# Kernel optimization log

Measured on AMD Instinct MI355X. Metric: run time of the kernel, lower is better.

## Reference

```python
import jax, jax.numpy as jnp
import numpy as np

EPS = 1e-6


def setup_inputs() -> dict:
    key = jax.random.key(0)
    ks = jax.random.split(key, 7)
    T, B, D, N = 512, 32, 1024, 128
    scale_w = (6.0 / (N + D)) ** 0.5  # xavier_uniform bound
    def w(k):
        return jax.random.uniform(k, (N, D), jnp.float32, -scale_w, scale_w)
    return {
        "x": jax.random.normal(ks[0], (T, B, D), jnp.float32),
        "S0": jnp.zeros((B, N, N), jnp.float32),
        "W_k": w(ks[1]),
        "W_v": w(ks[2]),
        "W_q": w(ks[3]),
        "W_erase": w(ks[4]),
        "W_write": w(ks[5]),
    }


def _ntm_forward(x, S0, W_k, W_v, W_q, W_erase, W_write):
    # Projections for all timesteps at once: (T, B, n_state)
    k = jnp.einsum('tbd,nd->tbn', x, W_k)
    v = jnp.einsum('tbd,nd->tbn', x, W_v)
    q = jnp.einsum('tbd,nd->tbn', x, W_q)
    erase = jnp.einsum('tbd,nd->tbn', x, W_erase)  # use_sigmoid=False: raw
    write = jnp.einsum('tbd,nd->tbn', x, W_write)

    def step(S, inp):
        k_t, v_t, q_t, e_t, w_t = inp
        k_norm = k_t / (jnp.linalg.norm(k_t, axis=-1, keepdims=True) + EPS)
        # S: (B, n, n); outer products via broadcasting
        erase_outer = e_t[:, :, None] * k_norm[:, None, :]
        write_outer = (w_t * v_t)[:, :, None] * k_norm[:, None, :]
        S_new = jnp.tanh(S * (1.0 - erase_outer) + write_outer)
        Sq = jnp.einsum('bij,bj->bi', S_new, q_t)
        out = Sq * jax.nn.silu(Sq)
        return S_new, out

    S_final, outputs = jax.lax.scan(step, S0, (k, v, q, erase, write))
    return outputs, S_final


def reference(x, S0, W_k, W_v, W_q, W_erase, W_write):
    return _ntm_forward(x, S0, W_k, W_v, W_q, W_erase, W_write)
```

## Files before the change

kernel.cpp:

```cpp
#include <hip/hip_runtime.h>
#include <hip/hip_bf16.h>


typedef __attribute__((ext_vector_type(8))) short bf16x8;
typedef __attribute__((ext_vector_type(4))) float f32x4;
typedef __attribute__((ext_vector_type(2))) float f32x2;
typedef __attribute__((ext_vector_type(4))) unsigned short u16x4;
typedef __attribute__((ext_vector_type(8))) unsigned short u16x8;

static constexpr int T_STEPS = 512;
static constexpr int BATCH   = 32;
static constexpr int DDIM    = 1024;
static constexpr int NDIM    = 128;
static constexpr int LDC     = 5 * NDIM;
static constexpr int MROWS   = T_STEPS * BATCH;
static constexpr int OUT_N   = T_STEPS * BATCH * NDIM;

static constexpr size_t C_BYTES = (size_t)MROWS * LDC * 4;

__device__ __forceinline__ unsigned short rne_bf16(float v) {
    unsigned u = __builtin_bit_cast(unsigned, v);
    u += 0x7FFFu + ((u >> 16) & 1u);
    return (unsigned short)(u >> 16);
}

__global__ __launch_bounds__(256) void wconv_kernel(
    const float* __restrict__ w0, const float* __restrict__ w1,
    const float* __restrict__ w2, const float* __restrict__ w3,
    const float* __restrict__ w4,
    unsigned short* __restrict__ W2)
{
    const int idx = blockIdx.x * 256 + threadIdx.x;
    const size_t e = (size_t)idx * 4;
    const int bn = (int)(e >> 17);
    const int r  = (int)(e & 131071);
    const int n  = r >> 10;
    const int k  = r & 1023;

    const float* wp = w0;
    if (bn == 1) wp = w1;
    else if (bn == 2) wp = w2;
    else if (bn == 3) wp = w3;
    else if (bn == 4) wp = w4;

    f32x4 v = *(const f32x4*)(wp + r);
    u16x4 h;
#pragma unroll
    for (int j = 0; j < 4; ++j) h[j] = rne_bf16(v[j]);

    const int kk   = k >> 5;
    const int quad = (k >> 3) & 3;
    const size_t off = ((((size_t)(bn * 32 + kk) * 128 + n) * 4 + quad) * 8) + (k & 7);
    *(u16x4*)(W2 + off) = h;
}

__global__ __launch_bounds__(512, 2) void gemm4_kernel(
    const float* __restrict__ x,
    const unsigned short* __restrict__ W2,
    float* __restrict__ C)
{
    __shared__ unsigned short lds[64 * 1024];

    const int m0   = blockIdx.x * 64;
    const int tid  = threadIdx.x;
    const int wave = tid >> 6, lane = tid & 63;
    const int quad = lane >> 4, l16 = lane & 15;

    {
        const int k8 = tid & 127;
        const int rb = tid >> 7;
#pragma unroll 4
        for (int it = 0; it < 16; ++it) {
            const int row = it * 4 + rb;
            const float* src = x + (size_t)(m0 + row) * DDIM + k8 * 8;
            f32x4 v0 = *(const f32x4*)src;
            f32x4 v1 = *(const f32x4*)(src + 4);
            u16x8 h;
            h[0] = rne_bf16(v0[0]); h[1] = rne_bf16(v0[1]);
            h[2] = rne_bf16(v0[2]); h[3] = rne_bf16(v0[3]);
            h[4] = rne_bf16(v1[0]); h[5] = rne_bf16(v1[1]);
            h[6] = rne_bf16(v1[2]); h[7] = rne_bf16(v1[3]);
            const int byteo = row * 2048 + ((k8 * 16) ^ ((row & 7) << 4));
            *(u16x8*)((char*)lds + byteo) = h;
        }
    }
    __syncthreads();

    f32x4 acc[5][4];
#pragma unroll
    for (int bn = 0; bn < 5; ++bn)
#pragma unroll
        for (int mi = 0; mi < 4; ++mi) acc[bn][mi] = (f32x4)(0.0f);

    const int aswz = (l16 & 7) << 4;
    const unsigned short* bp = W2 + ((size_t)((wave * 16 + l16) * 4 + quad)) * 8;

    auto LDA = [&](int mi, int kk) -> bf16x8 {
        const int byteo = (mi * 16 + l16) * 2048 + ((kk * 64 + quad * 16) ^ aswz);
        return *(const bf16x8*)((const char*)lds + byteo);
    };

    bf16x8 aC[4], bC[5], aN[4], bN[5];
#pragma unroll
    for (int mi = 0; mi < 4; ++mi) aC[mi] = LDA(mi, 0);
#pragma unroll
    for (int bn = 0; bn < 5; ++bn)
        bC[bn] = *(const bf16x8*)(bp + (size_t)bn * 131072);

    for (int kk = 0; kk < 32; kk += 2) {
#pragma unroll
        for (int mi = 0; mi < 4; ++mi) aN[mi] = LDA(mi, kk + 1);
#pragma unroll
        for (int bn = 0; bn < 5; ++bn)
            bN[bn] = *(const bf16x8*)(bp + (size_t)bn * 131072 + (size_t)(kk + 1) * 4096);
#pragma unroll
        for (int bn = 0; bn < 5; ++bn)
#pragma unroll
            for (int mi = 0; mi < 4; ++mi)
                acc[bn][mi] = __builtin_amdgcn_mfma_f32_16x16x32_bf16(
                    aC[mi], bC[bn], acc[bn][mi], 0, 0, 0);
        if (kk < 30) {
#pragma unroll
            for (int mi = 0; mi < 4; ++mi) aC[mi] = LDA(mi, kk + 2);
#pragma unroll
            for (int bn = 0; bn < 5; ++bn)
                bC[bn] = *(const bf16x8*)(bp + (size_t)bn * 131072 + (size_t)(kk + 2) * 4096);
        }
#pragma unroll
        for (int bn = 0; bn < 5; ++bn)
#pragma unroll
            for (int mi = 0; mi < 4; ++mi)
                acc[bn][mi] = __builtin_amdgcn_mfma_f32_16x16x32_bf16(
                    aN[mi], bN[bn], acc[bn][mi], 0, 0, 0);
    }

#pragma unroll
    for (int bn = 0; bn < 5; ++bn)
#pragma unroll
        for (int mi = 0; mi < 4; ++mi) {
            const int rw = m0 + mi * 16 + quad * 4;
            const int cl = bn * 128 + wave * 16 + l16;
#pragma unroll
            for (int r = 0; r < 4; ++r)
                C[(size_t)(rw + r) * LDC + cl] = acc[bn][mi][r];
        }
}

__global__ __launch_bounds__(256) void knorm_kernel(float* __restrict__ C)
{
    const int r    = blockIdx.x * 4 + (threadIdx.x >> 6);
    const int lane = threadIdx.x & 63;
    float* base = C + (size_t)r * LDC;

    f32x2 k2 = *(const f32x2*)(base + lane * 2);
    f32x2 v2 = *(const f32x2*)(base + NDIM + lane * 2);
    f32x2 w2 = *(const f32x2*)(base + 4 * NDIM + lane * 2);

    float ss = k2.x * k2.x + k2.y * k2.y;
#pragma unroll
    for (int off = 32; off >= 1; off >>= 1) ss += __shfl_xor(ss, off, 64);
    float inv = __builtin_amdgcn_rcpf(sqrtf(ss) + 1e-6f);

    f32x2 kn = {k2.x * inv, k2.y * inv};
    f32x2 wv = {v2.x * w2.x, v2.y * w2.y};
    *(f32x2*)(base + lane * 2) = kn;
    *(f32x2*)(base + NDIM + lane * 2) = wv;
}

__device__ __forceinline__ float tanh_fast(float xx) {
    float ex = __builtin_amdgcn_exp2f(xx * 2.8853900817779268f);
    float r  = __builtin_amdgcn_rcpf(ex + 1.0f);
    return fmaf(-2.0f, r, 1.0f);
}

template <int CTRL, int RMASK>
__device__ __forceinline__ float dpp_add(float x) {
    int yi = __builtin_amdgcn_update_dpp(
        0, __builtin_bit_cast(int, x), CTRL, RMASK, 0xF, true);
    return x + __builtin_bit_cast(float, yi);
}

__device__ __forceinline__ float dpp_reduce32(float x) {
    x = dpp_add<0xB1,  0xF>(x);
    x = dpp_add<0x4E,  0xF>(x);
    x = dpp_add<0x141, 0xF>(x);
    x = dpp_add<0x140, 0xF>(x);
    x = dpp_add<0x142, 0xA>(x);
    return x;
}

__global__ __launch_bounds__(256) void ntm_scan_kernel(
    const float* __restrict__ C, const float* __restrict__ S0,
    float* __restrict__ out)
{
    const int L    = blockIdx.x;
    const int b    = (L & 7) + 8 * ((L >> 3) & 3);
    const int row  = (L >> 5) * 8 + (threadIdx.x >> 5);
    const int g    = threadIdx.x & 31;
    const int col0 = g * 4;

    f32x4 S = *(const f32x4*)(S0 + ((size_t)b * NDIM + row) * NDIM + col0);

    const size_t STRIDE = (size_t)BATCH * LDC;
    const float* pb = C + (size_t)b * LDC;

    f32x4 kS[4], qS[4];
    float eS[4], wvS[4];

#pragma unroll
    for (int s = 0; s < 2; ++s) {
        const float* p = pb + (size_t)s * STRIDE;
        kS[s]  = *(const f32x4*)(p + col0);
        qS[s]  = *(const f32x4*)(p + 2 * NDIM + col0);
        eS[s]  = p[3 * NDIM + row];
        wvS[s] = p[NDIM + row];
    }

    float* op = out + (size_t)b * NDIM + row;

    for (int ti = 0; ti < T_STEPS / 4; ++ti) {
#pragma unroll
        for (int j = 0; j < 4; ++j) {
            const int t = ti * 4 + j;
            {
                int tp = t + 2;
                if (tp > T_STEPS - 1) tp = T_STEPS - 1;
                const float* p = pb + (size_t)tp * STRIDE;
                const int ps = (j + 2) & 3;
                kS[ps]  = *(const f32x4*)(p + col0);
                qS[ps]  = *(const f32x4*)(p + 2 * NDIM + col0);
                eS[ps]  = p[3 * NDIM + row];
                wvS[ps] = p[NDIM + row];
            }
            float dot = 0.0f;
#pragma unroll
            for (int u = 0; u < 4; ++u) {
                float t0  = fmaf(-eS[j], S[u], wvS[j]);
                float pre = fmaf(kS[j][u], t0, S[u]);
                S[u] = tanh_fast(pre);
                dot = fmaf(S[u], qS[j][u], dot);
            }
            dot = dpp_reduce32(dot);

            if ((threadIdx.x & 31) == 31) {
                const float d = dot;
                const float sg = __builtin_amdgcn_rcpf(
                    1.0f + __builtin_amdgcn_exp2f(-d * 1.4426950408889634f));
                op[(size_t)t * BATCH * NDIM] = d * d * sg;
            }
        }
    }

    *(f32x4*)(out + (size_t)T_STEPS * BATCH * NDIM
              + ((size_t)b * NDIM + row) * NDIM + col0) = S;
}

extern "C" void kernel_launch(void* const* d_in, const int* in_sizes, int n_in,
                              void* d_out, int out_size, void* d_ws, size_t ws_size,
                              hipStream_t stream) {
    const float* x  = (const float*)d_in[0];
    const float* S0 = (const float*)d_in[1];
    const float* wk = (const float*)d_in[2];
    const float* wv = (const float*)d_in[3];
    const float* wq = (const float*)d_in[4];
    const float* we = (const float*)d_in[5];
    const float* ww = (const float*)d_in[6];
    float* out = (float*)d_out;
    float* C   = (float*)d_ws;
    unsigned short* W2 = (unsigned short*)((char*)d_ws + C_BYTES);

    wconv_kernel<<<640, 256, 0, stream>>>(wk, wv, wq, we, ww, W2);
    gemm4_kernel<<<256, 512, 0, stream>>>(x, W2, C);
    knorm_kernel<<<MROWS / 4, 256, 0, stream>>>(C);
    ntm_scan_kernel<<<512, 256, 0, stream>>>(C, S0, out);
}
```

Measured before the change: 266.5 us.

## Split GEMM into column passes, move SiLU out of scan, simplify scan indexing

The projection GEMM now runs three sequential passes over 2, 2 and 1 column blocks, which cuts accumulator registers per pass at the cost of re-reading A from LDS three times. The scan kernel drops the per-step SiLU transcendental and the clamped prefetch index. It walks a running pointer instead and peels the last four steps, and it gets a two-blocks-per-SM launch bound. A separate elementwise kernel then applies d*d*sigmoid(d) to all outputs, which adds one extra read and write pass over the output.

```diff
diff --git a/kernel.cpp b/kernel.cpp
--- a/kernel.cpp
+++ b/kernel.cpp
@@ -54,7 +54,74 @@
     *(u16x4*)(W2 + off) = h;
 }
 
-__global__ __launch_bounds__(512, 2) void gemm4_kernel(
+template<int BN0, int NB>
+__device__ __forceinline__ void gemm_pass(
+    const unsigned short (&lds)[64 * 1024],
+    const unsigned short* __restrict__ bp,
+    float* __restrict__ C,
+    int m0, int wave, int quad, int l16, int aswz)
+{
+    auto LDA = [&](int mi, int kk) -> bf16x8 {
+        const int byteo = (mi * 16 + l16) * 2048 + ((kk * 64 + quad * 16) ^ aswz);
+        return *(const bf16x8*)((const char*)lds + byteo);
+    };
+
+    f32x4 acc[NB][4];
+#pragma unroll
+    for (int q = 0; q < NB; ++q)
+#pragma unroll
+        for (int mi = 0; mi < 4; ++mi) acc[q][mi] = (f32x4)(0.0f);
+
+    const unsigned short* bpp[NB];
+#pragma unroll
+    for (int q = 0; q < NB; ++q) bpp[q] = bp + (size_t)(BN0 + q) * 131072;
+
+    bf16x8 aC[4], bC[NB], aN[4], bN[NB];
+#pragma unroll
+    for (int mi = 0; mi < 4; ++mi) aC[mi] = LDA(mi, 0);
+#pragma unroll
+    for (int q = 0; q < NB; ++q) bC[q] = *(const bf16x8*)bpp[q];
+
+    for (int kk = 0; kk < 32; kk += 2) {
+#pragma unroll
+        for (int mi = 0; mi < 4; ++mi) aN[mi] = LDA(mi, kk + 1);
+#pragma unroll
+        for (int q = 0; q < NB; ++q)
+            bN[q] = *(const bf16x8*)(bpp[q] + (size_t)(kk + 1) * 4096);
+#pragma unroll
+        for (int q = 0; q < NB; ++q)
+#pragma unroll
+            for (int mi = 0; mi < 4; ++mi)
+                acc[q][mi] = __builtin_amdgcn_mfma_f32_16x16x32_bf16(
+                    aC[mi], bC[q], acc[q][mi], 0, 0, 0);
+        if (kk < 30) {
+#pragma unroll
+            for (int mi = 0; mi < 4; ++mi) aC[mi] = LDA(mi, kk + 2);
+#pragma unroll
+            for (int q = 0; q < NB; ++q)
+                bC[q] = *(const bf16x8*)(bpp[q] + (size_t)(kk + 2) * 4096);
+        }
+#pragma unroll
+        for (int q = 0; q < NB; ++q)
+#pragma unroll
+            for (int mi = 0; mi < 4; ++mi)
+                acc[q][mi] = __builtin_amdgcn_mfma_f32_16x16x32_bf16(
+                    aN[mi], bN[q], acc[q][mi], 0, 0, 0);
+    }
+
+#pragma unroll
+    for (int q = 0; q < NB; ++q)
+#pragma unroll
+        for (int mi = 0; mi < 4; ++mi) {
+            const int rw = m0 + mi * 16 + quad * 4;
+            const int cl = (BN0 + q) * 128 + wave * 16 + l16;
+#pragma unroll
+            for (int r = 0; r < 4; ++r)
+                C[(size_t)(rw + r) * LDC + cl] = acc[q][mi][r];
+        }
+}
+
+__global__ __launch_bounds__(512, 2) void gemm5_kernel(
     const float* __restrict__ x,
     const unsigned short* __restrict__ W2,
     float* __restrict__ C)
@@ -86,64 +153,12 @@
     }
     __syncthreads();
 
-    f32x4 acc[5][4];
-#pragma unroll
-    for (int bn = 0; bn < 5; ++bn)
-#pragma unroll
-        for (int mi = 0; mi < 4; ++mi) acc[bn][mi] = (f32x4)(0.0f);
-
     const int aswz = (l16 & 7) << 4;
     const unsigned short* bp = W2 + ((size_t)((wave * 16 + l16) * 4 + quad)) * 8;
 
-    auto LDA = [&](int mi, int kk) -> bf16x8 {
-        const int byteo = (mi * 16 + l16) * 2048 + ((kk * 64 + quad * 16) ^ aswz);
-        return *(const bf16x8*)((const char*)lds + byteo);
-    };
-
-    bf16x8 aC[4], bC[5], aN[4], bN[5];
-#pragma unroll
-    for (int mi = 0; mi < 4; ++mi) aC[mi] = LDA(mi, 0);
-#pragma unroll
-    for (int bn = 0; bn < 5; ++bn)
-        bC[bn] = *(const bf16x8*)(bp + (size_t)bn * 131072);
-
-    for (int kk = 0; kk < 32; kk += 2) {
-#pragma unroll
-        for (int mi = 0; mi < 4; ++mi) aN[mi] = LDA(mi, kk + 1);
-#pragma unroll
-        for (int bn = 0; bn < 5; ++bn)
-            bN[bn] = *(const bf16x8*)(bp + (size_t)bn * 131072 + (size_t)(kk + 1) * 4096);
-#pragma unroll
-        for (int bn = 0; bn < 5; ++bn)
-#pragma unroll
-            for (int mi = 0; mi < 4; ++mi)
-                acc[bn][mi] = __builtin_amdgcn_mfma_f32_16x16x32_bf16(
-                    aC[mi], bC[bn], acc[bn][mi], 0, 0, 0);
-        if (kk < 30) {
-#pragma unroll
-            for (int mi = 0; mi < 4; ++mi) aC[mi] = LDA(mi, kk + 2);
-#pragma unroll
-            for (int bn = 0; bn < 5; ++bn)
-                bC[bn] = *(const bf16x8*)(bp + (size_t)bn * 131072 + (size_t)(kk + 2) * 4096);
-        }
-#pragma unroll
-        for (int bn = 0; bn < 5; ++bn)
-#pragma unroll
-            for (int mi = 0; mi < 4; ++mi)
-                acc[bn][mi] = __builtin_amdgcn_mfma_f32_16x16x32_bf16(
-                    aN[mi], bN[bn], acc[bn][mi], 0, 0, 0);
-    }
-
-#pragma unroll
-    for (int bn = 0; bn < 5; ++bn)
-#pragma unroll
-        for (int mi = 0; mi < 4; ++mi) {
-            const int rw = m0 + mi * 16 + quad * 4;
-            const int cl = bn * 128 + wave * 16 + l16;
-#pragma unroll
-            for (int r = 0; r < 4; ++r)
-                C[(size_t)(rw + r) * LDC + cl] = acc[bn][mi][r];
-        }
+    gemm_pass<0, 2>(lds, bp, C, m0, wave, quad, l16, aswz);
+    gemm_pass<2, 2>(lds, bp, C, m0, wave, quad, l16, aswz);
+    gemm_pass<4, 1>(lds, bp, C, m0, wave, quad, l16, aswz);
 }
 
 __global__ __launch_bounds__(256) void knorm_kernel(float* __restrict__ C)
@@ -189,7 +204,7 @@
     return x;
 }
 
-__global__ __launch_bounds__(256) void ntm_scan_kernel(
+__global__ __launch_bounds__(256, 2) void ntm_scan_kernel(
     const float* __restrict__ C, const float* __restrict__ S0,
     float* __restrict__ out)
 {
@@ -216,22 +231,19 @@
         wvS[s] = p[NDIM + row];
     }
 
-    float* op = out + (size_t)b * NDIM + row;
-
-    for (int ti = 0; ti < T_STEPS / 4; ++ti) {
+    float* opc = out + (size_t)b * NDIM + row;
+    const float* pc = pb + 2 * STRIDE;
+
+    for (int ti = 0; ti < 127; ++ti) {
 #pragma unroll
         for (int j = 0; j < 4; ++j) {
-            const int t = ti * 4 + j;
-            {
-                int tp = t + 2;
-                if (tp > T_STEPS - 1) tp = T_STEPS - 1;
-                const float* p = pb + (size_t)tp * STRIDE;
-                const int ps = (j + 2) & 3;
-                kS[ps]  = *(const f32x4*)(p + col0);
-                qS[ps]  = *(const f32x4*)(p + 2 * NDIM + col0);
-                eS[ps]  = p[3 * NDIM + row];
-                wvS[ps] = p[NDIM + row];
-            }
+            const int ps = (j + 2) & 3;
+            kS[ps]  = *(const f32x4*)(pc + col0);
+            qS[ps]  = *(const f32x4*)(pc + 2 * NDIM + col0);
+            eS[ps]  = pc[3 * NDIM + row];
+            wvS[ps] = pc[NDIM + row];
+            pc += STRIDE;
+
             float dot = 0.0f;
 #pragma unroll
             for (int u = 0; u < 4; ++u) {
@@ -242,17 +254,54 @@
             }
             dot = dpp_reduce32(dot);
 
-            if ((threadIdx.x & 31) == 31) {
-                const float d = dot;
-                const float sg = __builtin_amdgcn_rcpf(
-                    1.0f + __builtin_amdgcn_exp2f(-d * 1.4426950408889634f));
-                op[(size_t)t * BATCH * NDIM] = d * d * sg;
-            }
-        }
+            if ((threadIdx.x & 31) == 31)
+                *opc = dot;
+            opc += BATCH * NDIM;
+        }
+    }
+
+#pragma unroll
+    for (int j = 0; j < 4; ++j) {
+        const int ps = (j + 2) & 3;
+        int tp = 510 + j;
+        if (tp > T_STEPS - 1) tp = T_STEPS - 1;
+        const float* p = pb + (size_t)tp * STRIDE;
+        kS[ps]  = *(const f32x4*)(p + col0);
+        qS[ps]  = *(const f32x4*)(p + 2 * NDIM + col0);
+        eS[ps]  = p[3 * NDIM + row];
+        wvS[ps] = p[NDIM + row];
+
+        float dot = 0.0f;
+#pragma unroll
+        for (int u = 0; u < 4; ++u) {
+            float t0  = fmaf(-eS[j], S[u], wvS[j]);
+            float pre = fmaf(kS[j][u], t0, S[u]);
+            S[u] = tanh_fast(pre);
+            dot = fmaf(S[u], qS[j][u], dot);
+        }
+        dot = dpp_reduce32(dot);
+
+        if ((threadIdx.x & 31) == 31)
+            *opc = dot;
+        opc += BATCH * NDIM;
     }
 
     *(f32x4*)(out + (size_t)T_STEPS * BATCH * NDIM
               + ((size_t)b * NDIM + row) * NDIM + col0) = S;
+}
+
+__global__ __launch_bounds__(256) void silu_kernel(float* __restrict__ out)
+{
+    const int i = blockIdx.x * 256 + threadIdx.x;
+    f32x4 d = ((const f32x4*)out)[i];
+    f32x4 y;
+#pragma unroll
+    for (int j = 0; j < 4; ++j) {
+        float sg = __builtin_amdgcn_rcpf(
+            1.0f + __builtin_amdgcn_exp2f(-d[j] * 1.4426950408889634f));
+        y[j] = d[j] * d[j] * sg;
+    }
+    ((f32x4*)out)[i] = y;
 }
 
 extern "C" void kernel_launch(void* const* d_in, const int* in_sizes, int n_in,
@@ -270,7 +319,8 @@
     unsigned short* W2 = (unsigned short*)((char*)d_ws + C_BYTES);
 
     wconv_kernel<<<640, 256, 0, stream>>>(wk, wv, wq, we, ww, W2);
-    gemm4_kernel<<<256, 512, 0, stream>>>(x, W2, C);
+    gemm5_kernel<<<256, 512, 0, stream>>>(x, W2, C);
     knorm_kernel<<<MROWS / 4, 256, 0, stream>>>(C);
     ntm_scan_kernel<<<512, 256, 0, stream>>>(C, S0, out);
-}
+    silu_kernel<<<OUT_N / 1024, 256, 0, stream>>>(out);
+}
```

Result: no change. 261.5 us (-1.9%).
